# Kernel optimization log

Hardware: AMD Instinct MI355X
Metric: run time of the kernel (lower is better)

## Reference

```python
import jax, jax.numpy as jnp
import numpy as np

B, N_CH, N_SMP = 8, 16, 480000   # batch, HOA channels (order 3), samples (10 s @ 48 kHz)
N_EARS, N_TAP = 2, 2048          # binaural ears, filter taps


def setup_inputs() -> dict:
    key = jax.random.key(0)
    k1, k2 = jax.random.split(key)
    hoa = jax.random.normal(k1, (B, N_CH, N_SMP), dtype=jnp.float32)
    # decoding filter buffer hoa2bin_t: [n_ears, n_ch, n_tap]
    hoa2bin_t = jax.random.normal(k2, (N_EARS, N_CH, N_TAP), dtype=jnp.float32)
    return {"hoa": hoa, "hoa2bin_t": hoa2bin_t}


def reference(hoa, hoa2bin_t):
    # Faithful to: sum_ch( fftconvolve(hoa[:,None], filt[None])[..., :-n_tap+1] )
    # Full linear convolution length:
    n_smp = hoa.shape[-1]
    n_tap = hoa2bin_t.shape[-1]
    L = n_smp + n_tap - 1
    Hf = jnp.fft.rfft(hoa, n=L, axis=-1)         # [B, n_ch, F] complex
    Gf = jnp.fft.rfft(hoa2bin_t, n=L, axis=-1)   # [E, n_ch, F] complex
    # Exploit FFT linearity: accumulate over channels in frequency domain,
    # then a single inverse FFT per (batch, ear). Same math as conv-then-sum.
    Yf = jnp.einsum('bcf,ecf->bef', Hf, Gf)      # [B, E, F]
    y = jnp.fft.irfft(Yf, n=L, axis=-1)          # [B, E, L]
    # slice [..., :-n_tap+1] of the full conv == first n_smp samples
    return y[..., :n_smp]
```

## Files before the change

### kernel.cpp

```cpp
#include <hip/hip_runtime.h>
#include <hip/hip_bf16.h>

#define N_BATCH 8
#define N_CH    16
#define N_SMP   480000
#define N_EARS  2
#define N_TAP   2048

#define NKT     65
#define ROWS    256
#define N_QROWS (N_SMP / 16)
#define QB_PER_B ((N_QROWS + ROWS - 1) / ROWS)
#define XS_LEN  6400
#define NF4     (XS_LEN / 4)
#define BLK     256
#define BQD     6

typedef __bf16 bf16x8 __attribute__((ext_vector_type(8)));
typedef float  f32x4  __attribute__((ext_vector_type(4)));

__global__ void build_bpk(const float* __restrict__ h, __bf16* __restrict__ bpk)
{
    const int idx = blockIdx.x * 256 + threadIdx.x;
    const int total = N_CH * NKT * 2 * 64 * 8;
    if (idx >= total) return;

    const int j    = idx & 7;
    const int lane = (idx >> 3) & 63;
    const int e    = (idx >> 9) & 1;
    const int ckt  = idx >> 10;
    const int kt   = ckt % NKT;
    const int c    = ckt / NKT;

    const int n  = lane & 15;
    const int kq = (lane >> 4) * 8 + j;
    const int u  = kt * 32 + kq;
    const int k  = 2048 - u + n;

    float val = (k >= 0 && k < N_TAP) ? h[((long)e * N_CH + c) * N_TAP + k] : 0.0f;
    bpk[idx] = (__bf16)val;
}

__global__ __launch_bounds__(BLK, 2)
void hoa_bin_gemm(const float* __restrict__ hoa,
                  const __bf16* __restrict__ bpk,
                  float* __restrict__ out)
{
    __shared__ __align__(16) __bf16 xs[2][XS_LEN];

    const int qb   = blockIdx.x;
    const int b    = blockIdx.y;
    const int tid  = threadIdx.x;
    const int lane = tid & 63;
    const int wv   = tid >> 6;
    const int mlan = lane & 15;
    const int quad = lane >> 4;

    const int q0 = qb * ROWS;
    const int t0 = 16 * q0 - 2048;

    const int abase = wv * 1024 + 16 * mlan + 8 * quad;

    const float* xb = hoa + (long)b * N_CH * N_SMP;

    f32x4 acc[4][2] = {};

    {
        float4 v[7];
        #pragma unroll
        for (int k = 0; k < 7; ++k) {
            const int i4 = tid + k * BLK;
            const int t  = t0 + 4 * i4;
            float4 w = {0.f, 0.f, 0.f, 0.f};
            if (i4 < NF4 && t >= 0 && t <= N_SMP - 4) w = *(const float4*)(xb + t);
            v[k] = w;
        }
        #pragma unroll
        for (int k = 0; k < 7; ++k) {
            const int i4 = tid + k * BLK;
            if (i4 < NF4) {
                union { __bf16 hh[4]; uint2 u; } pk;
                pk.hh[0] = (__bf16)v[k].x; pk.hh[1] = (__bf16)v[k].y;
                pk.hh[2] = (__bf16)v[k].z; pk.hh[3] = (__bf16)v[k].w;
                *(uint2*)(&xs[0][4 * i4]) = pk.u;
            }
        }
    }

    for (int c = 0; c < N_CH; ++c) {
        const __bf16* bp = bpk + (long)c * (NKT * 1024) + lane * 8;

        bf16x8 BQ0[BQD], BQ1[BQD];
        #pragma unroll
        for (int d = 0; d < BQD; ++d) {
            BQ0[d] = *(const bf16x8*)(bp + d * 1024);
            BQ1[d] = *(const bf16x8*)(bp + d * 1024 + 512);
        }

        __syncthreads();

        const __bf16* xw = &xs[c & 1][0];

        bf16x8 W[4][8];
        #pragma unroll
        for (int i = 0; i < 8; ++i)
            #pragma unroll
            for (int s = 0; s < 4; ++s)
                W[s][i] = *(const bf16x8*)(xw + abase + 32 * (8 * s + i));

        float4 sreg[7];

        #pragma unroll
        for (int g = 0; g < 8; ++g) {
            const int g4 = g & 3;
            #pragma unroll
            for (int i = 0; i < 8; ++i) {
                const int kt = 8 * g + i;
                const int d  = kt % BQD;
                bf16x8 b0 = BQ0[d];
                bf16x8 b1 = BQ1[d];
                const int ktp = (kt + BQD <= 64) ? kt + BQD : 64;
                BQ0[d] = *(const bf16x8*)(bp + ktp * 1024);
                BQ1[d] = *(const bf16x8*)(bp + ktp * 1024 + 512);
                __builtin_amdgcn_s_setprio(1);
                #pragma unroll
                for (int s = 0; s < 4; ++s) {
                    acc[s][0] = __builtin_amdgcn_mfma_f32_16x16x32_bf16(
                                    W[(g4 + s) & 3][i], b0, acc[s][0], 0, 0, 0);
                    acc[s][1] = __builtin_amdgcn_mfma_f32_16x16x32_bf16(
                                    W[(g4 + s) & 3][i], b1, acc[s][1], 0, 0, 0);
                }
                __builtin_amdgcn_s_setprio(0);
                W[g4][i] = *(const bf16x8*)(xw + abase + 32 * (8 * g + 32 + i));
            }
            if (g == 1 && c + 1 < N_CH) {
                const float* xc = xb + (long)(c + 1) * N_SMP;
                #pragma unroll
                for (int k = 0; k < 7; ++k) {
                    const int i4 = tid + k * BLK;
                    const int t  = t0 + 4 * i4;
                    float4 w = {0.f, 0.f, 0.f, 0.f};
                    if (i4 < NF4 && t >= 0 && t <= N_SMP - 4) w = *(const float4*)(xc + t);
                    sreg[k] = w;
                }
            }
        }

        {
            bf16x8 b0 = BQ0[64 % BQD];
            bf16x8 b1 = BQ1[64 % BQD];
            __builtin_amdgcn_s_setprio(1);
            #pragma unroll
            for (int s = 0; s < 4; ++s) {
                acc[s][0] = __builtin_amdgcn_mfma_f32_16x16x32_bf16(
                                W[s][0], b0, acc[s][0], 0, 0, 0);
                acc[s][1] = __builtin_amdgcn_mfma_f32_16x16x32_bf16(
                                W[s][0], b1, acc[s][1], 0, 0, 0);
            }
            __builtin_amdgcn_s_setprio(0);
        }

        if (c + 1 < N_CH) {
            __bf16* xd = &xs[(c + 1) & 1][0];
            #pragma unroll
            for (int k = 0; k < 7; ++k) {
                const int i4 = tid + k * BLK;
                if (i4 < NF4) {
                    union { __bf16 hh[4]; uint2 u; } pk;
                    pk.hh[0] = (__bf16)sreg[k].x; pk.hh[1] = (__bf16)sreg[k].y;
                    pk.hh[2] = (__bf16)sreg[k].z; pk.hh[3] = (__bf16)sreg[k].w;
                    *(uint2*)(&xd[4 * i4]) = pk.u;
                }
            }
        }
    }

    const long ob = (long)b * N_EARS * N_SMP;
    #pragma unroll
    for (int s = 0; s < 4; ++s) {
        #pragma unroll
        for (int e = 0; e < N_EARS; ++e) {
            #pragma unroll
            for (int r = 0; r < 4; ++r) {
                const int rl = wv * 64 + s * 16 + quad * 4 + r;
                const int q  = q0 + rl;
                if (q < N_QROWS)
                    out[ob + (long)e * N_SMP + 16 * q + mlan] = acc[s][e][r];
            }
        }
    }
}

extern "C" void kernel_launch(void* const* d_in, const int* in_sizes, int n_in,
                              void* d_out, int out_size, void* d_ws, size_t ws_size,
                              hipStream_t stream)
{
    const float* hoa = (const float*)d_in[0];
    const float* h   = (const float*)d_in[1];
    float* out       = (float*)d_out;
    __bf16* bpk      = (__bf16*)d_ws;

    const int total_bpk = N_CH * NKT * 2 * 64 * 8;
    build_bpk<<<(total_bpk + 255) / 256, 256, 0, stream>>>(h, bpk);

    dim3 grid(QB_PER_B, N_BATCH);
    hoa_bin_gemm<<<grid, BLK, 0, stream>>>(hoa, bpk, out);
}
```

Before: 737.3 us.

## Load signal windows directly from global memory, dropping LDS staging and barriers

Removes the double-buffered shared-memory staging of each channel's bf16 signal window and the per-channel __syncthreads. Each lane now loads its 8-sample A fragments straight from global memory (two float4 loads plus conversion) and zeroes them outside the valid range. The filter prefetch depth drops from 6 to 3 to free registers. This removes barrier and LDS traffic, but global loads become redundant: overlapping windows are re-read through cache by many lanes and waves, and the global-load latency now sits directly in the MFMA loop.

```diff
diff --git a/kernel.cpp b/kernel.cpp
--- a/kernel.cpp
+++ b/kernel.cpp
@@ -11,10 +11,8 @@
 #define ROWS    256
 #define N_QROWS (N_SMP / 16)
 #define QB_PER_B ((N_QROWS + ROWS - 1) / ROWS)
-#define XS_LEN  6400
-#define NF4     (XS_LEN / 4)
 #define BLK     256
-#define BQD     6
+#define BQD     3
 
 typedef __bf16 bf16x8 __attribute__((ext_vector_type(8)));
 typedef float  f32x4  __attribute__((ext_vector_type(4)));
@@ -41,13 +39,26 @@
     bpk[idx] = (__bf16)val;
 }
 
+__device__ __forceinline__ bf16x8 ldf(const float* __restrict__ x, int t)
+{
+    int tc = t < 0 ? 0 : t;
+    tc = tc > (N_SMP - 8) ? (N_SMP - 8) : tc;
+    const float4 a  = *(const float4*)(x + tc);
+    const float4 b2 = *(const float4*)(x + tc + 4);
+    union { __bf16 h[8]; bf16x8 v; } r;
+    r.h[0] = (__bf16)a.x;  r.h[1] = (__bf16)a.y;
+    r.h[2] = (__bf16)a.z;  r.h[3] = (__bf16)a.w;
+    r.h[4] = (__bf16)b2.x; r.h[5] = (__bf16)b2.y;
+    r.h[6] = (__bf16)b2.z; r.h[7] = (__bf16)b2.w;
+    const bf16x8 z = {};
+    return (t == tc) ? r.v : z;
+}
+
 __global__ __launch_bounds__(BLK, 2)
 void hoa_bin_gemm(const float* __restrict__ hoa,
                   const __bf16* __restrict__ bpk,
                   float* __restrict__ out)
 {
-    __shared__ __align__(16) __bf16 xs[2][XS_LEN];
-
     const int qb   = blockIdx.x;
     const int b    = blockIdx.y;
     const int tid  = threadIdx.x;
@@ -60,35 +71,15 @@
     const int t0 = 16 * q0 - 2048;
 
     const int abase = wv * 1024 + 16 * mlan + 8 * quad;
+    const int tw    = t0 + abase;
 
     const float* xb = hoa + (long)b * N_CH * N_SMP;
 
     f32x4 acc[4][2] = {};
 
-    {
-        float4 v[7];
-        #pragma unroll
-        for (int k = 0; k < 7; ++k) {
-            const int i4 = tid + k * BLK;
-            const int t  = t0 + 4 * i4;
-            float4 w = {0.f, 0.f, 0.f, 0.f};
-            if (i4 < NF4 && t >= 0 && t <= N_SMP - 4) w = *(const float4*)(xb + t);
-            v[k] = w;
-        }
-        #pragma unroll
-        for (int k = 0; k < 7; ++k) {
-            const int i4 = tid + k * BLK;
-            if (i4 < NF4) {
-                union { __bf16 hh[4]; uint2 u; } pk;
-                pk.hh[0] = (__bf16)v[k].x; pk.hh[1] = (__bf16)v[k].y;
-                pk.hh[2] = (__bf16)v[k].z; pk.hh[3] = (__bf16)v[k].w;
-                *(uint2*)(&xs[0][4 * i4]) = pk.u;
-            }
-        }
-    }
-
     for (int c = 0; c < N_CH; ++c) {
         const __bf16* bp = bpk + (long)c * (NKT * 1024) + lane * 8;
+        const float*  xc = xb + (long)c * N_SMP;
 
         bf16x8 BQ0[BQD], BQ1[BQD];
         #pragma unroll
@@ -97,18 +88,12 @@
             BQ1[d] = *(const bf16x8*)(bp + d * 1024 + 512);
         }
 
-        __syncthreads();
-
-        const __bf16* xw = &xs[c & 1][0];
-
         bf16x8 W[4][8];
         #pragma unroll
-        for (int i = 0; i < 8; ++i)
+        for (int s = 0; s < 4; ++s)
             #pragma unroll
-            for (int s = 0; s < 4; ++s)
-                W[s][i] = *(const bf16x8*)(xw + abase + 32 * (8 * s + i));
-
-        float4 sreg[7];
+            for (int i = 0; i < 8; ++i)
+                W[s][i] = ldf(xc, tw + 32 * (8 * s + i));
 
         #pragma unroll
         for (int g = 0; g < 8; ++g) {
@@ -131,18 +116,7 @@
                                     W[(g4 + s) & 3][i], b1, acc[s][1], 0, 0, 0);
                 }
                 __builtin_amdgcn_s_setprio(0);
-                W[g4][i] = *(const bf16x8*)(xw + abase + 32 * (8 * g + 32 + i));
-            }
-            if (g == 1 && c + 1 < N_CH) {
-                const float* xc = xb + (long)(c + 1) * N_SMP;
-                #pragma unroll
-                for (int k = 0; k < 7; ++k) {
-                    const int i4 = tid + k * BLK;
-                    const int t  = t0 + 4 * i4;
-                    float4 w = {0.f, 0.f, 0.f, 0.f};
-                    if (i4 < NF4 && t >= 0 && t <= N_SMP - 4) w = *(const float4*)(xc + t);
-                    sreg[k] = w;
-                }
+                W[g4][i] = ldf(xc, tw + 32 * (8 * g + 32 + i));
             }
         }
 
@@ -158,20 +132,6 @@
                                 W[s][0], b1, acc[s][1], 0, 0, 0);
             }
             __builtin_amdgcn_s_setprio(0);
-        }
-
-        if (c + 1 < N_CH) {
-            __bf16* xd = &xs[(c + 1) & 1][0];
-            #pragma unroll
-            for (int k = 0; k < 7; ++k) {
-                const int i4 = tid + k * BLK;
-                if (i4 < NF4) {
-                    union { __bf16 hh[4]; uint2 u; } pk;
-                    pk.hh[0] = (__bf16)sreg[k].x; pk.hh[1] = (__bf16)sreg[k].y;
-                    pk.hh[2] = (__bf16)sreg[k].z; pk.hh[3] = (__bf16)sreg[k].w;
-                    *(uint2*)(&xd[4 * i4]) = pk.u;
-                }
-            }
         }
     }
 
```

Result: slower. 2.126 ms (+188.3%).
